# Kernel optimization log

Hardware: AMD Instinct MI355X
Metric: run time of the kernel (lower is better)

The kernel has to match this reference:

```python
import jax, jax.numpy as jnp
import numpy as np

DIM = 96
NUM_EXPERTS = 4
TOP_K = 1

def setup_inputs() -> dict:
    key = jax.random.key(0)
    ks = jax.random.split(key, 8)
    B, C, H, W = 16, DIM, 128, 128
    E = NUM_EXPERTS
    x = jax.random.normal(ks[0], (B, C, H, W), dtype=jnp.float32)
    # per-expert depthwise 3x3 conv (groups=C): torch weight [C,1,3,3]
    dw_w = jax.random.normal(ks[1], (E, C, 1, 3, 3), dtype=jnp.float32) * 0.1
    dw_b = jax.random.normal(ks[2], (E, C), dtype=jnp.float32) * 0.05
    # per-expert pointwise 1x1 conv: torch weight [C,C,1,1]
    pw_w = jax.random.normal(ks[3], (E, C, C, 1, 1), dtype=jnp.float32) * 0.1
    pw_b = jax.random.normal(ks[4], (E, C), dtype=jnp.float32) * 0.05
    # router linear: torch weight [E, C]
    router_w = jax.random.normal(ks[5], (E, C), dtype=jnp.float32) * 0.1
    router_b = jax.random.normal(ks[6], (E,), dtype=jnp.float32) * 0.05
    return {"x": x, "dw_w": dw_w, "dw_b": dw_b, "pw_w": pw_w, "pw_b": pw_b,
            "router_w": router_w, "router_b": router_b}

def _conv(x, w, groups):
    return jax.lax.conv_general_dilated(
        x, w, window_strides=(1, 1), padding='SAME',
        dimension_numbers=('NCHW', 'OIHW', 'NCHW'),
        feature_group_count=groups)

def _expert(x, dw_w, dw_b, pw_w, pw_b):
    C = x.shape[1]
    h = _conv(x, dw_w, groups=C) + dw_b[None, :, None, None]   # depthwise 3x3
    h = jax.nn.gelu(h, approximate=False)                       # torch GELU (erf)
    return _conv(h, pw_w, groups=1) + pw_b[None, :, None, None] # 1x1 conv

def reference(x, dw_w, dw_b, pw_w, pw_b, router_w, router_b):
    B, C, H, W = x.shape
    E = dw_w.shape[0]
    # router: global avg pool -> linear -> softmax
    pooled = jnp.mean(x, axis=(2, 3))                            # [B, C]
    logits = pooled @ router_w.T + router_b                      # [B, E]
    router_weights = jax.nn.softmax(logits, axis=-1)
    top_weights, top_indices = jax.lax.top_k(router_weights, TOP_K)  # [B, k]
    top_weights = top_weights / (jnp.sum(top_weights, axis=-1, keepdims=True) + 1e-8)
    # run all experts (faithful to the original, which does not dispatch)
    expert_outputs = jnp.stack(
        [_expert(x, dw_w[e], dw_b[e], pw_w[e], pw_b[e]) for e in range(E)],
        axis=1)                                                  # [B, E, C, H, W]
    # scatter top-k weights into dense gates [B, E]
    gates = jnp.zeros((B, E), dtype=x.dtype)
    gates = gates.at[jnp.arange(B)[:, None], top_indices].set(top_weights)
    return jnp.einsum('bechw,be->bchw', expert_outputs, gates)
```

## Files before the change

### kernel.cpp

```cpp
#include <hip/hip_runtime.h>
#include <math.h>

#define DIM 96
#define NE 4
#define HH 128
#define WW 128
#define BB 16
#define KP 24
#define HSROW (KP * 2)
#define HSBUF (WW * HSROW)
#define PWROW 192

typedef __attribute__((ext_vector_type(8))) __bf16 bf16x8;
typedef __attribute__((ext_vector_type(4))) float floatx4;

__device__ __forceinline__ unsigned short f2bf(float f) {
    unsigned u = __builtin_bit_cast(unsigned, f);
    unsigned r = u + 0x7FFFu + ((u >> 16) & 1u);
    return (unsigned short)(r >> 16);
}
__device__ __forceinline__ unsigned pack2(float a, float b) {
    return (unsigned)f2bf(a) | ((unsigned)f2bf(b) << 16);
}

__device__ __forceinline__ void barrier_lds_only() {
    asm volatile("s_waitcnt lgkmcnt(0)" ::: "memory");
    __builtin_amdgcn_s_barrier();
}

__device__ __forceinline__ float gelu_erf(float h) {
    const float x = h * 0.70710678118654752f;
    const float a = fabsf(x);
    const float t = __builtin_amdgcn_rcpf(__builtin_fmaf(0.3275911f, a, 1.0f));
    float p = __builtin_fmaf(1.061405429f, t, -1.453152027f);
    p = __builtin_fmaf(p, t, 1.421413741f);
    p = __builtin_fmaf(p, t, -0.284496736f);
    p = __builtin_fmaf(p, t, 0.254829592f);
    p *= t;
    const float e = __expf(-x * x);
    float erfv = __builtin_fmaf(-p, e, 1.0f);
    erfv = copysignf(erfv, x);
    return 0.5f * h * (1.0f + erfv);
}

__global__ __launch_bounds__(256) void pool_kernel(const float* __restrict__ x,
                                                   float* __restrict__ pooled) {
    const int bc = blockIdx.x;
    const float4* p = (const float4*)(x + (size_t)bc * (HH * WW));
    const int t = threadIdx.x;
    float s = 0.f;
#pragma unroll
    for (int k = 0; k < (HH * WW / 4) / 256; ++k) {
        float4 v = p[t + k * 256];
        s += v.x + v.y + v.z + v.w;
    }
#pragma unroll
    for (int off = 32; off; off >>= 1) s += __shfl_down(s, off, 64);
    __shared__ float ls[4];
    if ((t & 63) == 0) ls[t >> 6] = s;
    __syncthreads();
    if (t == 0) pooled[bc] = (ls[0] + ls[1] + ls[2] + ls[3]) * (1.0f / (HH * WW));
}

__global__ void router_kernel(const float* __restrict__ pooled,
                              const float* __restrict__ rw,
                              const float* __restrict__ rb,
                              float* __restrict__ gate, int* __restrict__ sel) {
    const int b = threadIdx.x;
    if (b >= BB) return;
    float logits[NE];
#pragma unroll
    for (int e = 0; e < NE; ++e) {
        float s = rb[e];
        for (int c = 0; c < DIM; ++c) s += pooled[b * DIM + c] * rw[e * DIM + c];
        logits[e] = s;
    }
    float m = logits[0];
    int mi = 0;
#pragma unroll
    for (int e = 1; e < NE; ++e)
        if (logits[e] > m) { m = logits[e]; mi = e; }
    float denom = 0.f;
#pragma unroll
    for (int e = 0; e < NE; ++e) denom += expf(logits[e] - m);
    float w = 1.0f / denom;
    gate[b] = w / (w + 1e-8f);
    sel[b] = mi;
}

__device__ __forceinline__ void issue_sub(const float* __restrict__ x, int b,
                                          int cbase, int cg, int rr0, int r,
                                          int rr2, int p4, float4 f[2][3]) {
#pragma unroll
    for (int u = 0; u < 2; ++u) {
        const float* pl = x + (size_t)(b * DIM + cbase + cg * 2 + u) * (HH * WW);
        f[u][0] = *(const float4*)(pl + rr0 * WW + p4);
        f[u][1] = *(const float4*)(pl + r   * WW + p4);
        f[u][2] = *(const float4*)(pl + rr2 * WW + p4);
    }
}

__device__ __forceinline__ void compute_sub(const float4 f[2][3],
                                            const float (*dwc)[12], int cb,
                                            int cg, float lmask, float rmask,
                                            unsigned char* hsbuf, int p4,
                                            unsigned swz) {
    float hq[2][4];
#pragma unroll
    for (int u = 0; u < 2; ++u) {
        const int c = cb + cg * 2 + u;
        const float4 wA = *(const float4*)&dwc[c][0];
        const float4 wB = *(const float4*)&dwc[c][4];
        const float4 wC = *(const float4*)&dwc[c][8];
        float h0 = wC.y, h1 = wC.y, h2 = wC.y, h3 = wC.y;
#pragma unroll
        for (int row = 0; row < 3; ++row) {
            const float ta = (row == 0) ? wA.x : ((row == 1) ? wA.w : wB.z);
            const float tb = (row == 0) ? wA.y : ((row == 1) ? wB.x : wB.w);
            const float tc = (row == 0) ? wA.z : ((row == 1) ? wB.y : wC.x);
            const float4 f4 = f[u][row];
            const float vl = __shfl_up(f4.w, 1, 32) * lmask;
            const float vr = __shfl_down(f4.x, 1, 32) * rmask;
            h0 = __builtin_fmaf(ta, vl,   __builtin_fmaf(tb, f4.x, __builtin_fmaf(tc, f4.y, h0)));
            h1 = __builtin_fmaf(ta, f4.x, __builtin_fmaf(tb, f4.y, __builtin_fmaf(tc, f4.z, h1)));
            h2 = __builtin_fmaf(ta, f4.y, __builtin_fmaf(tb, f4.z, __builtin_fmaf(tc, f4.w, h2)));
            h3 = __builtin_fmaf(ta, f4.z, __builtin_fmaf(tb, f4.w, __builtin_fmaf(tc, vr, h3)));
        }
        hq[u][0] = gelu_erf(h0);
        hq[u][1] = gelu_erf(h1);
        hq[u][2] = gelu_erf(h2);
        hq[u][3] = gelu_erf(h3);
    }
    const unsigned wb0 = (unsigned)(p4 * HSROW + cg * 4);
#pragma unroll
    for (int j = 0; j < 4; ++j) {
        const unsigned off = (wb0 + (unsigned)j * HSROW) ^ swz;
        *(unsigned*)(hsbuf + off) = pack2(hq[0][j], hq[1][j]);
    }
}

__global__ __launch_bounds__(256, 3) void moe_main(
    const float* __restrict__ x, const float* __restrict__ dw_w,
    const float* __restrict__ dw_b, const float* __restrict__ pw_w,
    const float* __restrict__ pw_b, const float* __restrict__ gate,
    const int* __restrict__ sel, float* __restrict__ out) {
    __shared__ __align__(16) unsigned char pwb[DIM * PWROW];
    __shared__ __align__(16) unsigned char hsb[4 * HSBUF];
    __shared__ float dwc[DIM][12];

    const int t = threadIdx.x;
    const unsigned bid = blockIdx.x;
    const int xcd = bid & 7;
    const int s = bid >> 3;
    const int b = s & 15;
    const int r = xcd * 16 + (s >> 4);
    const int e = sel[b];
    const float g = gate[b];

    const int lane = t & 63, w = t >> 6;
    const int wm = w & 1, wn = w >> 1;
    const int ln = lane & 15, kg = lane >> 4;
    const int cobase = wm * 48, pxbase = wn * 64;

    const int g32 = t & 31;
    const int p4 = g32 * 4;
    const int cg = t >> 5;
    const unsigned swz = (unsigned)((g32 & 7) << 4);
    const float lmask = (p4 == 0) ? 0.f : 1.f;
    const float rmask = (p4 == 124) ? 0.f : 1.f;

    const float m0 = (r > 0) ? 1.f : 0.f;
    const float m2 = (r < HH - 1) ? 1.f : 0.f;
    const int rr0 = (r > 0) ? r - 1 : 0;
    const int rr2 = (r < HH - 1) ? r + 1 : HH - 1;

    float4 fA[2][3], fB[2][3];
    issue_sub(x, b, 0, cg, rr0, r, rr2, p4, fA);
    issue_sub(x, b, 16, cg, rr0, r, rr2, p4, fB);

#pragma unroll
    for (int i = 0; i < 18; ++i) {
        const int u = i * 256 + t;
        const int co = u / 48, kp = u - co * 48;
        const float2 v = *(const float2*)(pw_w +
            ((size_t)e * DIM + co) * DIM + kp * 2);
        *(unsigned*)(pwb + ((unsigned)(co * PWROW + kp * 4) ^
                            (unsigned)((co & 7) << 4))) = pack2(v.x, v.y);
    }
    for (int j = t; j < DIM * 12; j += 256) {
        const int c = j / 12, q = j - c * 12;
        float v = 0.f;
        if (q < 9) {
            v = dw_w[((size_t)e * DIM + c) * 9 + q];
            if (q < 3) v *= m0;
            if (q >= 6) v *= m2;
        } else if (q == 9) v = dw_b[e * DIM + c];
        dwc[c][q] = v;
    }
    barrier_lds_only();

    floatx4 acc[3][4];
#pragma unroll
    for (int i = 0; i < 3; ++i)
#pragma unroll
        for (int j = 0; j < 4; ++j) acc[i][j] = (floatx4){0.f, 0.f, 0.f, 0.f};

#pragma unroll
    for (int pair = 0; pair < 3; ++pair) {
        const int cb = pair * 32;
        unsigned char* h0 = hsb + (unsigned)((pair & 1) * 2) * HSBUF;
        unsigned char* h1 = h0 + HSBUF;
        compute_sub(fA, dwc, cb, cg, lmask, rmask, h0, p4, swz);
        if (pair < 2) issue_sub(x, b, cb + 32, cg, rr0, r, rr2, p4, fA);
        compute_sub(fB, dwc, cb + 16, cg, lmask, rmask, h1, p4, swz);
        if (pair < 2) issue_sub(x, b, cb + 48, cg, rr0, r, rr2, p4, fB);
        barrier_lds_only();

        const unsigned qbase = (unsigned)((pair & 1) * 2 + (kg >> 1)) * HSBUF;
        bf16x8 af[3], bfr[4];
#pragma unroll
        for (int mf = 0; mf < 3; ++mf) {
            const int co = cobase + mf * 16 + ln;
            af[mf] = *(const bf16x8*)(pwb +
                ((unsigned)(co * PWROW + pair * 64 + kg * 16) ^
                 (unsigned)((co & 7) << 4)));
        }
#pragma unroll
        for (int nf = 0; nf < 4; ++nf) {
            const int pxv = pxbase + nf * 16 + ln;
            const unsigned boff = (unsigned)((pxv * HSROW + (kg & 1) * 16) ^
                                             (((pxv >> 2) & 7) << 4));
            bfr[nf] = *(const bf16x8*)(hsb + qbase + boff);
        }
#pragma unroll
        for (int mf = 0; mf < 3; ++mf)
#pragma unroll
            for (int nf = 0; nf < 4; ++nf)
                acc[mf][nf] = __builtin_amdgcn_mfma_f32_16x16x32_bf16(
                    af[mf], bfr[nf], acc[mf][nf], 0, 0, 0);
    }

#pragma unroll
    for (int mf = 0; mf < 3; ++mf) {
#pragma unroll
        for (int rr = 0; rr < 4; ++rr) {
            const int co = cobase + mf * 16 + kg * 4 + rr;
            const float bias = pw_b[e * DIM + co];
            float* orow = out + ((size_t)(b * DIM + co) * HH + r) * WW;
#pragma unroll
            for (int nf = 0; nf < 4; ++nf)
                orow[pxbase + nf * 16 + ln] = (acc[mf][nf][rr] + bias) * g;
        }
    }
}

extern "C" void kernel_launch(void* const* d_in, const int* in_sizes, int n_in,
                              void* d_out, int out_size, void* d_ws, size_t ws_size,
                              hipStream_t stream) {
    const float* x    = (const float*)d_in[0];
    const float* dw_w = (const float*)d_in[1];
    const float* dw_b = (const float*)d_in[2];
    const float* pw_w = (const float*)d_in[3];
    const float* pw_b = (const float*)d_in[4];
    const float* rw   = (const float*)d_in[5];
    const float* rb   = (const float*)d_in[6];
    float* out = (float*)d_out;

    float* pooled = (float*)d_ws;
    float* gate = pooled + BB * DIM;
    int* sel = (int*)(gate + BB);

    pool_kernel<<<BB * DIM, 256, 0, stream>>>(x, pooled);
    router_kernel<<<1, 64, 0, stream>>>(pooled, rw, rb, gate, sel);
    moe_main<<<HH * BB, 256, 0, stream>>>(x, dw_w, dw_b, pw_w, pw_b, gate, sel, out);
}
```

Measured before the change: 76.76 us.

## Fuse router into main kernel and remap blocks to batch-per-XCD

```diff
diff --git a/kernel.cpp b/kernel.cpp
--- a/kernel.cpp
+++ b/kernel.cpp
@@ -62,32 +62,6 @@
     if (t == 0) pooled[bc] = (ls[0] + ls[1] + ls[2] + ls[3]) * (1.0f / (HH * WW));
 }
 
-__global__ void router_kernel(const float* __restrict__ pooled,
-                              const float* __restrict__ rw,
-                              const float* __restrict__ rb,
-                              float* __restrict__ gate, int* __restrict__ sel) {
-    const int b = threadIdx.x;
-    if (b >= BB) return;
-    float logits[NE];
-#pragma unroll
-    for (int e = 0; e < NE; ++e) {
-        float s = rb[e];
-        for (int c = 0; c < DIM; ++c) s += pooled[b * DIM + c] * rw[e * DIM + c];
-        logits[e] = s;
-    }
-    float m = logits[0];
-    int mi = 0;
-#pragma unroll
-    for (int e = 1; e < NE; ++e)
-        if (logits[e] > m) { m = logits[e]; mi = e; }
-    float denom = 0.f;
-#pragma unroll
-    for (int e = 0; e < NE; ++e) denom += expf(logits[e] - m);
-    float w = 1.0f / denom;
-    gate[b] = w / (w + 1e-8f);
-    sel[b] = mi;
-}
-
 __device__ __forceinline__ void issue_sub(const float* __restrict__ x, int b,
                                           int cbase, int cg, int rr0, int r,
                                           int rr2, int p4, float4 f[2][3]) {
@@ -142,20 +116,20 @@
 __global__ __launch_bounds__(256, 3) void moe_main(
     const float* __restrict__ x, const float* __restrict__ dw_w,
     const float* __restrict__ dw_b, const float* __restrict__ pw_w,
-    const float* __restrict__ pw_b, const float* __restrict__ gate,
-    const int* __restrict__ sel, float* __restrict__ out) {
+    const float* __restrict__ pw_b, const float* __restrict__ pooled,
+    const float* __restrict__ rw, const float* __restrict__ rb,
+    float* __restrict__ out) {
     __shared__ __align__(16) unsigned char pwb[DIM * PWROW];
     __shared__ __align__(16) unsigned char hsb[4 * HSBUF];
     __shared__ float dwc[DIM][12];
+    __shared__ float lsm[4];
 
     const int t = threadIdx.x;
     const unsigned bid = blockIdx.x;
     const int xcd = bid & 7;
     const int s = bid >> 3;
-    const int b = s & 15;
-    const int r = xcd * 16 + (s >> 4);
-    const int e = sel[b];
-    const float g = gate[b];
+    const int b = xcd * 2 + (s >> 7);
+    const int r = s & 127;
 
     const int lane = t & 63, w = t >> 6;
     const int wm = w & 1, wn = w >> 1;
@@ -177,6 +151,30 @@
     float4 fA[2][3], fB[2][3];
     issue_sub(x, b, 0, cg, rr0, r, rr2, p4, fA);
     issue_sub(x, b, 16, cg, rr0, r, rr2, p4, fB);
+
+    {
+        float part = pooled[b * DIM + lane] * rw[w * DIM + lane];
+        if (lane < 32)
+            part += pooled[b * DIM + 64 + lane] * rw[w * DIM + 64 + lane];
+#pragma unroll
+        for (int off = 32; off; off >>= 1) part += __shfl_down(part, off, 64);
+        if (lane == 0) lsm[w] = part + rb[w];
+    }
+    barrier_lds_only();
+    int e;
+    float g;
+    {
+        const float l0 = lsm[0], l1 = lsm[1], l2 = lsm[2], l3 = lsm[3];
+        float m = l0; int mi = 0;
+        if (l1 > m) { m = l1; mi = 1; }
+        if (l2 > m) { m = l2; mi = 2; }
+        if (l3 > m) { m = l3; mi = 3; }
+        const float denom = __expf(l0 - m) + __expf(l1 - m) +
+                            __expf(l2 - m) + __expf(l3 - m);
+        const float wv = 1.0f / denom;
+        g = wv / (wv + 1e-8f);
+        e = mi;
+    }
 
 #pragma unroll
     for (int i = 0; i < 18; ++i) {
@@ -267,10 +265,8 @@
     float* out = (float*)d_out;
 
     float* pooled = (float*)d_ws;
-    float* gate = pooled + BB * DIM;
-    int* sel = (int*)(gate + BB);
 
     pool_kernel<<<BB * DIM, 256, 0, stream>>>(x, pooled);
-    router_kernel<<<1, 64, 0, stream>>>(pooled, rw, rb, gate, sel);
-    moe_main<<<HH * BB, 256, 0, stream>>>(x, dw_w, dw_b, pw_w, pw_b, gate, sel, out);
-}
+    moe_main<<<HH * BB, 256, 0, stream>>>(x, dw_w, dw_b, pw_w, pw_b,
+                                          pooled, rw, rb, out);
+}
```

Measured after the change: 67.22 us. -12.4%, faster.
